# Performance work log

Hardware: AMD Instinct MI355X
Metric: run time of the kernel (lower is better)

Reference implementation:

```python
import jax, jax.numpy as jnp
import numpy as np

N_EXPERTS = 8
TOP_K = 2
D_MODEL = 4096
RANK = 64


def setup_inputs() -> dict:
    key = jax.random.key(0)
    k0, k1, k2, k3 = jax.random.split(key, 4)
    inputs = jax.random.normal(k0, (4, 2048, D_MODEL), dtype=jnp.float32)
    gate_w = jax.random.normal(k1, (N_EXPERTS, D_MODEL), dtype=jnp.float32) * 0.02
    lora_A = jax.random.normal(k2, (N_EXPERTS, RANK, D_MODEL), dtype=jnp.float32) * 0.02
    lora_B = jax.random.normal(k3, (N_EXPERTS, D_MODEL, RANK), dtype=jnp.float32) * 0.02
    return {"inputs": inputs, "gate_w": gate_w, "lora_A": lora_A, "lora_B": lora_B}


def reference(inputs, gate_w, lora_A, lora_B):
    # Flatten tokens: [B, S, D] -> [T, D]
    x = inputs.reshape(-1, inputs.shape[-1])
    T = x.shape[0]
    # Softmax gate over experts: [T, E]
    gate_probs = jax.nn.softmax(x @ gate_w.T, axis=-1)
    # Top-k selection + renormalization of routing weights
    weights, sel = jax.lax.top_k(gate_probs, TOP_K)          # [T, k]
    weights = weights / jnp.sum(weights, axis=-1, keepdims=True)
    # Scatter top-k weights into dense combine matrix [T, E]
    w_full = jnp.zeros((T, N_EXPERTS), dtype=x.dtype).at[
        jnp.arange(T)[:, None], sel
    ].add(weights)
    # Per-expert LoRA FFN: y_e = (x @ A_e^T) @ B_e^T, combined with routing weights
    out = jnp.zeros((T, D_MODEL), dtype=x.dtype)
    for e in range(N_EXPERTS):
        y = (x @ lora_A[e].T) @ lora_B[e].T                  # [T, D]
        out = out + w_full[:, e:e + 1] * y
    return out.reshape(inputs.shape[:-1] + (D_MODEL,))
```

## Files before the change

kernel.cpp:

```cpp
#include <hip/hip_runtime.h>
#include <hip/hip_bf16.h>
#include <cstdint>
#include <cstddef>

#define T_TOKENS 8192
#define DM 4096
#define NE 8
#define RANK 64

#define WS_CNT 0
#define WS_LISTS 1024
#define WS_WTS (WS_LISTS + 2 * 8 * 8192 * 4)
#define WS_SELP (WS_WTS + 8192 * 2 * 4)
#define WS_ZPART (1 << 20)
#define WS_ZBF (10 << 20)
#define ZP (8192 * 2 * 64)

typedef __attribute__((ext_vector_type(8))) short bfrag;
typedef __attribute__((ext_vector_type(4))) float f4acc;

__device__ __forceinline__ unsigned short f2bf(float f) {
    unsigned int u = __float_as_uint(f);
    return (unsigned short)((u + 0x7FFF + ((u >> 16) & 1)) >> 16);
}

__global__ __launch_bounds__(256) void gate_kernel(
    const float* __restrict__ x, const float* __restrict__ gw,
    unsigned short* __restrict__ selp, float* __restrict__ wts) {
    int tid = threadIdx.x;
    int wave = tid >> 6, lane = tid & 63;
    int t0 = blockIdx.x * 4;

    float acc[4][8];
#pragma unroll
    for (int tt = 0; tt < 4; ++tt)
#pragma unroll
        for (int e = 0; e < 8; ++e) acc[tt][e] = 0.f;

    const float* xb = x + (size_t)t0 * DM + wave * 1024 + lane * 4;
    const float* gb = gw + wave * 1024 + lane * 4;
#pragma unroll 2
    for (int i = 0; i < 4; ++i) {
        float4 xv0 = *(const float4*)(xb + 0 * DM + i * 256);
        float4 xv1 = *(const float4*)(xb + 1 * DM + i * 256);
        float4 xv2 = *(const float4*)(xb + 2 * DM + i * 256);
        float4 xv3 = *(const float4*)(xb + 3 * DM + i * 256);
#pragma unroll
        for (int e = 0; e < 8; ++e) {
            float4 gv = *(const float4*)(gb + (size_t)e * DM + i * 256);
            acc[0][e] = fmaf(xv0.x, gv.x, acc[0][e]);
            acc[0][e] = fmaf(xv0.y, gv.y, acc[0][e]);
            acc[0][e] = fmaf(xv0.z, gv.z, acc[0][e]);
            acc[0][e] = fmaf(xv0.w, gv.w, acc[0][e]);
            acc[1][e] = fmaf(xv1.x, gv.x, acc[1][e]);
            acc[1][e] = fmaf(xv1.y, gv.y, acc[1][e]);
            acc[1][e] = fmaf(xv1.z, gv.z, acc[1][e]);
            acc[1][e] = fmaf(xv1.w, gv.w, acc[1][e]);
            acc[2][e] = fmaf(xv2.x, gv.x, acc[2][e]);
            acc[2][e] = fmaf(xv2.y, gv.y, acc[2][e]);
            acc[2][e] = fmaf(xv2.z, gv.z, acc[2][e]);
            acc[2][e] = fmaf(xv2.w, gv.w, acc[2][e]);
            acc[3][e] = fmaf(xv3.x, gv.x, acc[3][e]);
            acc[3][e] = fmaf(xv3.y, gv.y, acc[3][e]);
            acc[3][e] = fmaf(xv3.z, gv.z, acc[3][e]);
            acc[3][e] = fmaf(xv3.w, gv.w, acc[3][e]);
        }
    }

#pragma unroll
    for (int tt = 0; tt < 4; ++tt)
#pragma unroll
        for (int e = 0; e < 8; ++e) {
            float v = acc[tt][e];
            v += __shfl_xor(v, 1, 64);
            v += __shfl_xor(v, 2, 64);
            v += __shfl_xor(v, 4, 64);
            v += __shfl_xor(v, 8, 64);
            v += __shfl_xor(v, 16, 64);
            v += __shfl_xor(v, 32, 64);
            acc[tt][e] = v;
        }

    float l8[8];
#pragma unroll
    for (int e = 0; e < 8; ++e) {
        float v = acc[0][e];
        v = (lane == 1) ? acc[1][e] : v;
        v = (lane == 2) ? acc[2][e] : v;
        v = (lane == 3) ? acc[3][e] : v;
        l8[e] = v;
    }

    __shared__ float part[4][4][8];
    if (lane < 4) {
#pragma unroll
        for (int e = 0; e < 8; ++e) part[wave][lane][e] = l8[e];
    }
    __syncthreads();

    if (tid < 4) {
        int t = t0 + tid;
        float s8[8];
#pragma unroll
        for (int e = 0; e < 8; ++e)
            s8[e] = ((part[0][tid][e] + part[1][tid][e]) +
                     (part[2][tid][e] + part[3][tid][e]));
        float m = s8[0];
#pragma unroll
        for (int j = 1; j < 8; ++j) m = fmaxf(m, s8[j]);
        float p[8];
#pragma unroll
        for (int j = 0; j < 8; ++j) p[j] = expf(s8[j] - m);
        int e0 = 0;
        float p0 = p[0];
#pragma unroll
        for (int j = 1; j < 8; ++j)
            if (p[j] > p0) { p0 = p[j]; e0 = j; }
        int e1 = -1;
        float p1 = -1.0f;
#pragma unroll
        for (int j = 0; j < 8; ++j)
            if (j != e0 && p[j] > p1) { p1 = p[j]; e1 = j; }
        float inv = 1.0f / (p0 + p1);
        wts[t * 2 + 0] = p0 * inv;
        wts[t * 2 + 1] = p1 * inv;
        selp[t] = (unsigned short)(e0 | (e1 << 8));
    }
}

__global__ __launch_bounds__(256) void build_lists(
    const unsigned short* __restrict__ selp,
    int* __restrict__ cnt, int* __restrict__ lists) {
    int b = blockIdx.x;
    int slot = b >> 3, e = b & 7;
    __shared__ int base;
    if (threadIdx.x == 0) base = 0;
    __syncthreads();
    int lane = threadIdx.x & 63, wv = threadIdx.x >> 6;
    int* listp = lists + b * T_TOKENS;
    int shift = slot * 8;
    for (int it = 0; it < T_TOKENS / 256; ++it) {
        int t = it * 256 + wv * 64 + lane;
        int ev = (selp[t] >> shift) & 255;
        bool mt = (ev == e);
        unsigned long long mask = __ballot(mt);
        int cw = __popcll(mask);
        int wbase = 0;
        if (lane == 0 && cw) wbase = atomicAdd(&base, cw);
        wbase = __shfl(wbase, 0, 64);
        if (mt) {
            int pos = __popcll(mask & ((1ull << lane) - 1ull));
            listp[wbase + pos] = t;
        }
    }
    __syncthreads();
    if (threadIdx.x == 0) cnt[b] = base;
}

#define TILES_A 20
#define BKA 128
#define PITCH_A 136
__global__ __launch_bounds__(256) void lora_a_mfma(
    const float* __restrict__ x, const float* __restrict__ A,
    const int* __restrict__ cnt, const int* __restrict__ lists,
    float* __restrict__ zpart) {
    int e = blockIdx.y;
    int sk = blockIdx.z;
    int slot = sk >> 1, kh = sk & 1;
    int count = cnt[slot * 8 + e];

    __shared__ __attribute__((aligned(16))) unsigned short xs[64 * PITCH_A];
    __shared__ __attribute__((aligned(16))) unsigned short as[64 * PITCH_A];
    __shared__ int stok[64];

    int tid = threadIdx.x;
    int wave = tid >> 6, lane = tid & 63;
    int q = lane >> 4, col = lane & 15;
    int srow = tid >> 2, sc = tid & 3;
    const int listbase = (slot * 8 + e) * T_TOKENS;
    float* zout = zpart + (size_t)kh * ZP;

    for (int ti = blockIdx.x; ti * 64 < count; ti += TILES_A) {
        int t0 = ti * 64;
        __syncthreads();
        if (tid < 64) {
            int idx = t0 + tid;
            stok[tid] = (idx < count) ? lists[listbase + idx] : lists[listbase];
        }
        __syncthreads();

        const float* xrow = x + (size_t)stok[srow] * DM + kh * 2048 + sc * 32;
        const float* arow = A + ((size_t)e * RANK + srow) * DM + kh * 2048 + sc * 32;

        f4acc acc[4] = {};

        for (int kb = 0; kb < 2048; kb += BKA) {
            __syncthreads();
#pragma unroll
            for (int j = 0; j < 4; ++j) {
                float4 v0 = *(const float4*)(xrow + kb + j * 8);
                float4 v1 = *(const float4*)(xrow + kb + j * 8 + 4);
                unsigned short tmp[8] = {f2bf(v0.x), f2bf(v0.y), f2bf(v0.z), f2bf(v0.w),
                                         f2bf(v1.x), f2bf(v1.y), f2bf(v1.z), f2bf(v1.w)};
                *(bfrag*)&xs[srow * PITCH_A + sc * 32 + j * 8] = *(bfrag*)tmp;
                float4 w0 = *(const float4*)(arow + kb + j * 8);
                float4 w1 = *(const float4*)(arow + kb + j * 8 + 4);
                unsigned short tm2[8] = {f2bf(w0.x), f2bf(w0.y), f2bf(w0.z), f2bf(w0.w),
                                         f2bf(w1.x), f2bf(w1.y), f2bf(w1.z), f2bf(w1.w)};
                *(bfrag*)&as[srow * PITCH_A + sc * 32 + j * 8] = *(bfrag*)tm2;
            }
            __syncthreads();
#pragma unroll
            for (int ks = 0; ks < BKA / 32; ++ks) {
                bfrag af = *(const bfrag*)&xs[(wave * 16 + col) * PITCH_A + ks * 32 + q * 8];
#pragma unroll
                for (int nt = 0; nt < 4; ++nt) {
                    bfrag bf = *(const bfrag*)&as[(nt * 16 + col) * PITCH_A + ks * 32 + q * 8];
                    acc[nt] = __builtin_amdgcn_mfma_f32_16x16x32_bf16(af, bf, acc[nt], 0, 0, 0);
                }
            }
        }
#pragma unroll
        for (int nt = 0; nt < 4; ++nt) {
#pragma unroll
            for (int r = 0; r < 4; ++r) {
                int mm = wave * 16 + q * 4 + r;
                if (t0 + mm < count) {
                    int tk = stok[mm];
                    zout[((size_t)tk * 2 + slot) * RANK + nt * 16 + col] = acc[nt][r];
                }
            }
        }
    }
}

__global__ __launch_bounds__(256) void zreduce_kernel(
    const float* __restrict__ zpart, const float* __restrict__ wts,
    unsigned short* __restrict__ zbf) {
    int i = blockIdx.x * 256 + threadIdx.x;
    float4 a = ((const float4*)zpart)[i];
    float4 b = ((const float4*)(zpart + ZP))[i];
    float w = wts[i >> 4];
    ushort4 o;
    o.x = f2bf((a.x + b.x) * w);
    o.y = f2bf((a.y + b.y) * w);
    o.z = f2bf((a.z + b.z) * w);
    o.w = f2bf((a.w + b.w) * w);
    ((ushort4*)zbf)[i] = o;
}

#define TILES_B2 16
#define PITCH_B 72
__global__ __launch_bounds__(256) void lora_b_mfma(
    const unsigned short* __restrict__ zbf, const float* __restrict__ B,
    const int* __restrict__ cnt, const int* __restrict__ lists,
    float* __restrict__ out, int slot) {
    int e = blockIdx.z;
    int count = cnt[slot * 8 + e];
    int d0 = blockIdx.x * 128;

    __shared__ __attribute__((aligned(16))) unsigned short zs[64 * PITCH_B];
    __shared__ __attribute__((aligned(16))) unsigned short bs[128 * PITCH_B];
    __shared__ int stok[64];

    int tid = threadIdx.x;
    int wave = tid >> 6, lane = tid & 63;
    int q = lane >> 4, col = lane & 15;
    const int listbase = (slot * 8 + e) * T_TOKENS;

    {
        int row = tid >> 1, h = tid & 1;
        const float* bp = B + ((size_t)e * DM + d0 + row) * RANK + h * 32;
#pragma unroll
        for (int j = 0; j < 4; ++j) {
            float4 v0 = *(const float4*)(bp + j * 8);
            float4 v1 = *(const float4*)(bp + j * 8 + 4);
            unsigned short tmp[8] = {f2bf(v0.x), f2bf(v0.y), f2bf(v0.z), f2bf(v0.w),
                                     f2bf(v1.x), f2bf(v1.y), f2bf(v1.z), f2bf(v1.w)};
            *(bfrag*)&bs[row * PITCH_B + h * 32 + j * 8] = *(bfrag*)tmp;
        }
    }

    for (int ti = blockIdx.y; ti * 64 < count; ti += TILES_B2) {
        int t0 = ti * 64;
        __syncthreads();
        if (tid < 64) {
            int idx = t0 + tid;
            stok[tid] = (idx < count) ? lists[listbase + idx] : -1;
        }
        __syncthreads();
        {
            int row = tid >> 2, c = tid & 3;
            int tk = stok[row];
            int tkc = tk < 0 ? 0 : tk;
            const uint4* zp = (const uint4*)(zbf + ((size_t)tkc * 2 + slot) * RANK + c * 16);
            uint4 v0 = zp[0];
            uint4 v1 = zp[1];
            *(uint4*)&zs[row * PITCH_B + c * 16] = v0;
            *(uint4*)&zs[row * PITCH_B + c * 16 + 8] = v1;
        }
        __syncthreads();

        f4acc acc[8] = {};
#pragma unroll
        for (int ks = 0; ks < 2; ++ks) {
            bfrag af = *(const bfrag*)&zs[(wave * 16 + col) * PITCH_B + ks * 32 + q * 8];
#pragma unroll
            for (int nt = 0; nt < 8; ++nt) {
                bfrag bf = *(const bfrag*)&bs[(nt * 16 + col) * PITCH_B + ks * 32 + q * 8];
                acc[nt] = __builtin_amdgcn_mfma_f32_16x16x32_bf16(af, bf, acc[nt], 0, 0, 0);
            }
        }
#pragma unroll
        for (int r = 0; r < 4; ++r) {
            int mm = wave * 16 + q * 4 + r;
            int tk = stok[mm];
            if (tk >= 0) {
                float* op = out + (size_t)tk * DM + d0 + col;
                if (slot == 0) {
#pragma unroll
                    for (int nt = 0; nt < 8; ++nt) op[nt * 16] = acc[nt][r];
                } else {
#pragma unroll
                    for (int nt = 0; nt < 8; ++nt) op[nt * 16] += acc[nt][r];
                }
            }
        }
    }
}

extern "C" void kernel_launch(void* const* d_in, const int* in_sizes, int n_in,
                              void* d_out, int out_size, void* d_ws, size_t ws_size,
                              hipStream_t stream) {
    const float* x = (const float*)d_in[0];
    const float* gw = (const float*)d_in[1];
    const float* A = (const float*)d_in[2];
    const float* Bm = (const float*)d_in[3];
    float* out = (float*)d_out;
    char* ws = (char*)d_ws;
    int* cnt = (int*)(ws + WS_CNT);
    int* lists = (int*)(ws + WS_LISTS);
    float* wts = (float*)(ws + WS_WTS);
    unsigned short* selp = (unsigned short*)(ws + WS_SELP);
    float* zpart = (float*)(ws + WS_ZPART);
    unsigned short* zbf = (unsigned short*)(ws + WS_ZBF);

    gate_kernel<<<2048, 256, 0, stream>>>(x, gw, selp, wts);
    build_lists<<<16, 256, 0, stream>>>(selp, cnt, lists);
    lora_a_mfma<<<dim3(TILES_A, 8, 4), 256, 0, stream>>>(x, A, cnt, lists, zpart);
    zreduce_kernel<<<1024, 256, 0, stream>>>(zpart, wts, zbf);
    lora_b_mfma<<<dim3(32, TILES_B2, 8), 256, 0, stream>>>(zbf, Bm, cnt, lists, out, 0);
    lora_b_mfma<<<dim3(32, TILES_B2, 8), 256, 0, stream>>>(zbf, Bm, cnt, lists, out, 1);
}
```

Baseline: 479.6 us.

## Pre-cast x, A, B to bf16 and use direct-to-LDS LoRA-A kernel

The gate kernel now also writes a bf16 copy of x, and a new cast kernel converts the A and B weights to bf16 once per call. A new LoRA-A kernel gathers routed tokens from bf16 x with global_load_lds into swizzled LDS, runs the full K reduction per tile, and applies routing weights directly. This removes the split-K partial buffer and the separate reduce kernel. The cost is an extra 64MB bf16 write of x plus a dependence on enough workspace, with a fallback to the old path when workspace is too small.

```diff
diff --git a/kernel.cpp b/kernel.cpp
--- a/kernel.cpp
+++ b/kernel.cpp
@@ -12,8 +12,12 @@
 #define WS_LISTS 1024
 #define WS_WTS (WS_LISTS + 2 * 8 * 8192 * 4)
 #define WS_SELP (WS_WTS + 8192 * 2 * 4)
+#define WS_ABF (1 << 20)
+#define WS_BBF (5 << 20)
 #define WS_ZPART (1 << 20)
 #define WS_ZBF (10 << 20)
+#define WS_XBF (12 << 20)
+#define WS_NEED_FAST ((size_t)(12 << 20) + (size_t)T_TOKENS * DM * 2)
 #define ZP (8192 * 2 * 64)
 
 typedef __attribute__((ext_vector_type(8))) short bfrag;
@@ -26,7 +30,8 @@
 
 __global__ __launch_bounds__(256) void gate_kernel(
     const float* __restrict__ x, const float* __restrict__ gw,
-    unsigned short* __restrict__ selp, float* __restrict__ wts) {
+    unsigned short* __restrict__ selp, float* __restrict__ wts,
+    unsigned short* __restrict__ xbf) {
     int tid = threadIdx.x;
     int wave = tid >> 6, lane = tid & 63;
     int t0 = blockIdx.x * 4;
@@ -45,6 +50,17 @@
         float4 xv1 = *(const float4*)(xb + 1 * DM + i * 256);
         float4 xv2 = *(const float4*)(xb + 2 * DM + i * 256);
         float4 xv3 = *(const float4*)(xb + 3 * DM + i * 256);
+        if (xbf) {
+            size_t xo = (size_t)t0 * DM + wave * 1024 + i * 256 + lane * 4;
+            ushort4 o0 = {f2bf(xv0.x), f2bf(xv0.y), f2bf(xv0.z), f2bf(xv0.w)};
+            ushort4 o1 = {f2bf(xv1.x), f2bf(xv1.y), f2bf(xv1.z), f2bf(xv1.w)};
+            ushort4 o2 = {f2bf(xv2.x), f2bf(xv2.y), f2bf(xv2.z), f2bf(xv2.w)};
+            ushort4 o3 = {f2bf(xv3.x), f2bf(xv3.y), f2bf(xv3.z), f2bf(xv3.w)};
+            *(ushort4*)(xbf + xo + 0 * DM) = o0;
+            *(ushort4*)(xbf + xo + 1 * DM) = o1;
+            *(ushort4*)(xbf + xo + 2 * DM) = o2;
+            *(ushort4*)(xbf + xo + 3 * DM) = o3;
+        }
 #pragma unroll
         for (int e = 0; e < 8; ++e) {
             float4 gv = *(const float4*)(gb + (size_t)e * DM + i * 256);
@@ -157,6 +173,99 @@
     if (threadIdx.x == 0) cnt[b] = base;
 }
 
+__global__ __launch_bounds__(256) void cast_ab(
+    const float* __restrict__ A, const float* __restrict__ B,
+    unsigned short* __restrict__ abf, unsigned short* __restrict__ bbf) {
+    size_t o = ((size_t)blockIdx.x * 256 + threadIdx.x) * 8;
+    float4 a0 = ((const float4*)(A + o))[0];
+    float4 a1 = ((const float4*)(A + o))[1];
+    unsigned short ta[8] = {f2bf(a0.x), f2bf(a0.y), f2bf(a0.z), f2bf(a0.w),
+                            f2bf(a1.x), f2bf(a1.y), f2bf(a1.z), f2bf(a1.w)};
+    *(bfrag*)(abf + o) = *(bfrag*)ta;
+    float4 b0 = ((const float4*)(B + o))[0];
+    float4 b1 = ((const float4*)(B + o))[1];
+    unsigned short tb[8] = {f2bf(b0.x), f2bf(b0.y), f2bf(b0.z), f2bf(b0.w),
+                            f2bf(b1.x), f2bf(b1.y), f2bf(b1.z), f2bf(b1.w)};
+    *(bfrag*)(bbf + o) = *(bfrag*)tb;
+}
+
+__global__ __launch_bounds__(256) void lora_a_v2(
+    const unsigned short* __restrict__ xbf, const unsigned short* __restrict__ abf,
+    const int* __restrict__ cnt, const int* __restrict__ lists,
+    const float* __restrict__ wts, unsigned short* __restrict__ zbf) {
+    int e = blockIdx.y, slot = blockIdx.z;
+    int count = cnt[slot * 8 + e];
+    int ti = blockIdx.x;
+    if (ti * 64 >= count) return;
+
+    __shared__ __attribute__((aligned(16))) unsigned short xs2[64 * 128];
+    __shared__ __attribute__((aligned(16))) unsigned short as2[64 * 128];
+    __shared__ int stok[64];
+    __shared__ float wv[64];
+
+    int tid = threadIdx.x;
+    int wave = tid >> 6, lane = tid & 63;
+    int q = lane >> 4, col = lane & 15;
+    const int listbase = (slot * 8 + e) * T_TOKENS;
+
+    if (tid < 64) {
+        int idx = ti * 64 + tid;
+        stok[tid] = (idx < count) ? lists[listbase + idx] : lists[listbase];
+    }
+    __syncthreads();
+    if (tid < 64) wv[tid] = wts[stok[tid] * 2 + slot];
+
+    const unsigned short* xg[4];
+    const unsigned short* ag[4];
+#pragma unroll
+    for (int i = 0; i < 4; ++i) {
+        int row = wave * 16 + i * 4 + (lane >> 4);
+        int koff = (((lane & 15) * 16) ^ ((row & 7) << 4)) >> 1;
+        xg[i] = xbf + (size_t)stok[row] * DM + koff;
+        ag[i] = abf + ((size_t)e * RANK + row) * DM + koff;
+    }
+
+    f4acc acc[4] = {};
+    const unsigned short* xrl = xs2 + (wave * 16 + col) * 128;
+    const unsigned short* arl = as2 + col * 128;
+    int sx = (col & 7) << 4;
+
+    for (int kb = 0; kb < DM; kb += 128) {
+        __syncthreads();
+#pragma unroll
+        for (int i = 0; i < 4; ++i) {
+            __builtin_amdgcn_global_load_lds(
+                (const unsigned int*)(xg[i] + kb),
+                (unsigned int*)&xs2[(wave * 16 + i * 4) * 128], 16, 0, 0);
+            __builtin_amdgcn_global_load_lds(
+                (const unsigned int*)(ag[i] + kb),
+                (unsigned int*)&as2[(wave * 16 + i * 4) * 128], 16, 0, 0);
+        }
+        __syncthreads();
+#pragma unroll
+        for (int ks = 0; ks < 4; ++ks) {
+            int off = ((ks * 64 + q * 16) ^ sx) >> 1;
+            bfrag af = *(const bfrag*)(xrl + off);
+#pragma unroll
+            for (int nt = 0; nt < 4; ++nt) {
+                bfrag bf = *(const bfrag*)(arl + nt * 2048 + off);
+                acc[nt] = __builtin_amdgcn_mfma_f32_16x16x32_bf16(af, bf, acc[nt], 0, 0, 0);
+            }
+        }
+    }
+#pragma unroll
+    for (int nt = 0; nt < 4; ++nt) {
+#pragma unroll
+        for (int r = 0; r < 4; ++r) {
+            int mm = wave * 16 + q * 4 + r;
+            if (ti * 64 + mm < count) {
+                zbf[((size_t)stok[mm] * 2 + slot) * RANK + nt * 16 + col] =
+                    f2bf(acc[nt][r] * wv[mm]);
+            }
+        }
+    }
+}
+
 #define TILES_A 20
 #define BKA 128
 #define PITCH_A 136
@@ -253,6 +362,7 @@
 #define PITCH_B 72
 __global__ __launch_bounds__(256) void lora_b_mfma(
     const unsigned short* __restrict__ zbf, const float* __restrict__ B,
+    const unsigned short* __restrict__ bbf,
     const int* __restrict__ cnt, const int* __restrict__ lists,
     float* __restrict__ out, int slot) {
     int e = blockIdx.z;
@@ -270,14 +380,23 @@
 
     {
         int row = tid >> 1, h = tid & 1;
-        const float* bp = B + ((size_t)e * DM + d0 + row) * RANK + h * 32;
-#pragma unroll
-        for (int j = 0; j < 4; ++j) {
-            float4 v0 = *(const float4*)(bp + j * 8);
-            float4 v1 = *(const float4*)(bp + j * 8 + 4);
-            unsigned short tmp[8] = {f2bf(v0.x), f2bf(v0.y), f2bf(v0.z), f2bf(v0.w),
-                                     f2bf(v1.x), f2bf(v1.y), f2bf(v1.z), f2bf(v1.w)};
-            *(bfrag*)&bs[row * PITCH_B + h * 32 + j * 8] = *(bfrag*)tmp;
+        if (bbf) {
+            const unsigned short* bp = bbf + ((size_t)e * DM + d0 + row) * RANK + h * 32;
+#pragma unroll
+            for (int j = 0; j < 4; ++j) {
+                bfrag v = *(const bfrag*)(bp + j * 8);
+                *(bfrag*)&bs[row * PITCH_B + h * 32 + j * 8] = v;
+            }
+        } else {
+            const float* bp = B + ((size_t)e * DM + d0 + row) * RANK + h * 32;
+#pragma unroll
+            for (int j = 0; j < 4; ++j) {
+                float4 v0 = *(const float4*)(bp + j * 8);
+                float4 v1 = *(const float4*)(bp + j * 8 + 4);
+                unsigned short tmp[8] = {f2bf(v0.x), f2bf(v0.y), f2bf(v0.z), f2bf(v0.w),
+                                         f2bf(v1.x), f2bf(v1.y), f2bf(v1.z), f2bf(v1.w)};
+                *(bfrag*)&bs[row * PITCH_B + h * 32 + j * 8] = *(bfrag*)tmp;
+            }
         }
     }
 
@@ -342,13 +461,25 @@
     int* lists = (int*)(ws + WS_LISTS);
     float* wts = (float*)(ws + WS_WTS);
     unsigned short* selp = (unsigned short*)(ws + WS_SELP);
-    float* zpart = (float*)(ws + WS_ZPART);
     unsigned short* zbf = (unsigned short*)(ws + WS_ZBF);
 
-    gate_kernel<<<2048, 256, 0, stream>>>(x, gw, selp, wts);
-    build_lists<<<16, 256, 0, stream>>>(selp, cnt, lists);
-    lora_a_mfma<<<dim3(TILES_A, 8, 4), 256, 0, stream>>>(x, A, cnt, lists, zpart);
-    zreduce_kernel<<<1024, 256, 0, stream>>>(zpart, wts, zbf);
-    lora_b_mfma<<<dim3(32, TILES_B2, 8), 256, 0, stream>>>(zbf, Bm, cnt, lists, out, 0);
-    lora_b_mfma<<<dim3(32, TILES_B2, 8), 256, 0, stream>>>(zbf, Bm, cnt, lists, out, 1);
-}
+    if (ws_size >= WS_NEED_FAST) {
+        unsigned short* abf = (unsigned short*)(ws + WS_ABF);
+        unsigned short* bbf = (unsigned short*)(ws + WS_BBF);
+        unsigned short* xbf = (unsigned short*)(ws + WS_XBF);
+        gate_kernel<<<2048, 256, 0, stream>>>(x, gw, selp, wts, xbf);
+        cast_ab<<<1024, 256, 0, stream>>>(A, Bm, abf, bbf);
+        build_lists<<<16, 256, 0, stream>>>(selp, cnt, lists);
+        lora_a_v2<<<dim3(128, 8, 2), 256, 0, stream>>>(xbf, abf, cnt, lists, wts, zbf);
+        lora_b_mfma<<<dim3(32, TILES_B2, 8), 256, 0, stream>>>(zbf, Bm, bbf, cnt, lists, out, 0);
+        lora_b_mfma<<<dim3(32, TILES_B2, 8), 256, 0, stream>>>(zbf, Bm, bbf, cnt, lists, out, 1);
+    } else {
+        float* zpart = (float*)(ws + WS_ZPART);
+        gate_kernel<<<2048, 256, 0, stream>>>(x, gw, selp, wts, nullptr);
+        build_lists<<<16, 256, 0, stream>>>(selp, cnt, lists);
+        lora_a_mfma<<<dim3(TILES_A, 8, 4), 256, 0, stream>>>(x, A, cnt, lists, zpart);
+        zreduce_kernel<<<1024, 256, 0, stream>>>(zpart, wts, zbf);
+        lora_b_mfma<<<dim3(32, TILES_B2, 8), 256, 0, stream>>>(zbf, Bm, nullptr, cnt, lists, out, 0);
+        lora_b_mfma<<<dim3(32, TILES_B2, 8), 256, 0, stream>>>(zbf, Bm, nullptr, cnt, lists, out, 1);
+    }
+}
```

After: 398.2 us. 1.2x faster.
